# Optimization experiments

Measured on AMD Instinct MI355X. Metric: run time of the kernel, lower is better.

## Reference

```python
import jax, jax.numpy as jnp
import numpy as np

B, N, QD = 2, 4096, 512
HEADS, DIM_HEAD = 8, 64
INNER = HEADS * DIM_HEAD  # 512
SCALE = DIM_HEAD ** -0.5


def setup_inputs() -> dict:
    key = jax.random.key(0)
    ks = jax.random.split(key, 6)
    s = 0.02
    return {
        "x": jax.random.normal(ks[0], (B, N, QD), dtype=jnp.float32),
        "Wq": jax.random.normal(ks[1], (QD, INNER), dtype=jnp.float32) * s,
        "Wk": jax.random.normal(ks[2], (QD, INNER), dtype=jnp.float32) * s,
        "Wv": jax.random.normal(ks[3], (QD, INNER), dtype=jnp.float32) * s,
        "Wo": jax.random.normal(ks[4], (INNER, QD), dtype=jnp.float32) * s,
        "bo": jnp.zeros((QD,), dtype=jnp.float32),
    }


def reference(x, Wq, Wk, Wv, Wo, bo):
    # self-attention: context = x; mask = None; attention_sf = False
    q = x @ Wq  # [B, N, INNER]
    k = x @ Wk
    v = x @ Wv
    # split heads: [B, H, N, D]
    def split(t):
        return t.reshape(B, N, HEADS, DIM_HEAD).transpose(0, 2, 1, 3)
    q, k, v = split(q), split(k), split(v)
    # fp32 QK^T (ATTN_PRECISION='fp32' path)
    sim = jnp.einsum('bhid,bhjd->bhij', q.astype(jnp.float32), k.astype(jnp.float32)) * SCALE
    attn = jax.nn.softmax(sim, axis=-1)
    out = jnp.einsum('bhij,bhjd->bhid', attn, v)  # [B, H, N, D]
    out = out.transpose(0, 2, 1, 3).reshape(B, N, INNER)
    return out @ Wo + bo  # Dropout(p=0) is identity
```

## Files before the change

### kernel.cpp

```cpp
#include <hip/hip_runtime.h>
#include <hip/hip_bf16.h>


typedef __attribute__((ext_vector_type(8))) short short8;
typedef __attribute__((ext_vector_type(4))) float floatx4;

#define MFMA16(a, b, c) __builtin_amdgcn_mfma_f32_16x16x32_bf16((a), (b), (c), 0, 0, 0)

#if __has_builtin(__builtin_amdgcn_exp2f)
#define EXP2(x) __builtin_amdgcn_exp2f(x)
#else
#define EXP2(x) exp2f(x)
#endif

#define QSCALE 0.18033688011112042f

static __device__ __forceinline__ unsigned short f2b(float f) {
  unsigned int u = __float_as_uint(f);
  u += 0x7FFFu + ((u >> 16) & 1u);
  return (unsigned short)(u >> 16);
}

static __device__ __forceinline__ unsigned int pkb(float a, float b) {
  float2 t{a, b};
  __hip_bfloat162 h = __float22bfloat162_rn(t);
  union { __hip_bfloat162 h2; unsigned int u; } cv;
  cv.h2 = h;
  return cv.u;
}

static __device__ __forceinline__ void dma16(const unsigned short* g,
                                             unsigned short* l) {
  __builtin_amdgcn_global_load_lds(
      (const __attribute__((address_space(1))) unsigned int*)g,
      (__attribute__((address_space(3))) unsigned int*)l, 16, 0, 0);
}

__global__ __launch_bounds__(256) void prep_kernel(
    const float* __restrict__ Wq, const float* __restrict__ Wk,
    const float* __restrict__ Wv, const float* __restrict__ Wo,
    const float* __restrict__ x, unsigned short* __restrict__ wtq,
    unsigned short* __restrict__ wtk, unsigned short* __restrict__ wtv,
    unsigned short* __restrict__ wto, unsigned short* __restrict__ xb) {
  const int z = blockIdx.z;
  const int tid = threadIdx.x;
  if (z >= 4) {
    const int bid = (z - 4) * 256 + blockIdx.y * 16 + blockIdx.x;
    const int idx = (bid * 256 + tid) * 8;
    const float4 a = *(const float4*)(x + idx);
    const float4 b = *(const float4*)(x + idx + 4);
    unsigned int u[4] = {pkb(a.x, a.y), pkb(a.z, a.w), pkb(b.x, b.y),
                         pkb(b.z, b.w)};
    *(short8*)(xb + idx) = *(short8*)u;
    return;
  }
  const float* __restrict__ W = (z == 0) ? Wq : (z == 1) ? Wk : (z == 2) ? Wv : Wo;
  unsigned short* __restrict__ T = (z == 0) ? wtq : (z == 1) ? wtk : (z == 2) ? wtv : wto;
  const int k0 = blockIdx.x * 32, c0 = blockIdx.y * 32;
  __shared__ float Ts[32][33];
  const int r = tid >> 3, cc = (tid & 7) * 4;
  const float4 v = *(const float4*)(W + (k0 + r) * 512 + c0 + cc);
  Ts[r][cc] = v.x; Ts[r][cc + 1] = v.y; Ts[r][cc + 2] = v.z; Ts[r][cc + 3] = v.w;
  __syncthreads();
  const unsigned long long uu =
      (unsigned long long)pkb(Ts[cc][r], Ts[cc + 1][r]) |
      ((unsigned long long)pkb(Ts[cc + 2][r], Ts[cc + 3][r]) << 32);
  *(unsigned long long*)(T + (c0 + r) * 512 + k0 + cc) = uu;
}

__global__ __launch_bounds__(256) void qkv_fused_kernel(
    const unsigned short* __restrict__ xb, const unsigned short* __restrict__ wtq,
    const unsigned short* __restrict__ wtk,
    const unsigned short* __restrict__ wtv, unsigned short* __restrict__ qo,
    unsigned short* __restrict__ ko, unsigned short* __restrict__ vo) {
  const int m0 = blockIdx.x * 128;
  const int c0 = blockIdx.y * 32;
  __shared__ __align__(16) unsigned short As[2][128 * 64];
  __shared__ __align__(16) unsigned short Bs[2][3][32 * 64];
  const int tid = threadIdx.x;
  const int lane = tid & 63, w = tid >> 6;
  const int i = lane & 15, q = lane >> 4;
  const int sl = i & 7;
  const int dr = lane >> 3, dc = lane & 7;
  const int sch = (dc ^ dr) * 8;
  const unsigned short* ag = xb + (m0 + w * 32 + dr) * 512 + sch;
  const unsigned short* bg[3];
  bg[0] = wtq + (c0 + w * 8 + dr) * 512 + sch;
  bg[1] = wtk + (c0 + w * 8 + dr) * 512 + sch;
  bg[2] = wtv + (c0 + w * 8 + dr) * 512 + sch;

  floatx4 acc[3][2][2] = {};

#pragma unroll
  for (int p = 0; p < 4; ++p) dma16(ag + p * 8 * 512, &As[0][(w * 32 + p * 8) * 64]);
#pragma unroll
  for (int z = 0; z < 3; ++z) dma16(bg[z], &Bs[0][z][(w * 8) * 64]);
  __syncthreads();

  int buf = 0;
  for (int ks = 0; ks < 8; ++ks) {
    if (ks < 7) {
      const int k1 = (ks + 1) * 64;
#pragma unroll
      for (int p = 0; p < 4; ++p)
        dma16(ag + p * 8 * 512 + k1, &As[buf ^ 1][(w * 32 + p * 8) * 64]);
#pragma unroll
      for (int z = 0; z < 3; ++z)
        dma16(bg[z] + k1, &Bs[buf ^ 1][z][(w * 8) * 64]);
    }
#pragma unroll
    for (int kc = 0; kc < 2; ++kc) {
      short8 af[2];
#pragma unroll
      for (int t = 0; t < 2; ++t)
        af[t] = *(const short8*)&As[buf][(w * 32 + t * 16 + i) * 64 +
                                        (((kc * 4 + q) ^ sl) * 8)];
#pragma unroll
      for (int z = 0; z < 3; ++z)
#pragma unroll
        for (int g = 0; g < 2; ++g) {
          const short8 bf = *(const short8*)&Bs[buf][z][(g * 16 + i) * 64 +
                                                        (((kc * 4 + q) ^ sl) * 8)];
#pragma unroll
          for (int t = 0; t < 2; ++t)
            acc[z][t][g] = MFMA16(af[t], bf, acc[z][t][g]);
        }
    }
    __syncthreads();
    buf ^= 1;
  }
#pragma unroll
  for (int z = 0; z < 3; ++z)
#pragma unroll
    for (int t = 0; t < 2; ++t)
#pragma unroll
      for (int g = 0; g < 2; ++g) {
        const int col = c0 + g * 16 + i;
        const int h = col >> 6, d = col & 63;
        const int row0 = m0 + w * 32 + t * 16 + q * 4;
        const int b = row0 >> 12;
        const int n0 = row0 & 4095;
        if (z == 2) {
          unsigned int* dst =
              (unsigned int*)&vo[(((b * 8 + h) * 64 + d) << 12) + n0];
          dst[0] = pkb(acc[z][t][g][0], acc[z][t][g][1]);
          dst[1] = pkb(acc[z][t][g][2], acc[z][t][g][3]);
        } else {
          unsigned short* dst = (z == 0) ? qo : ko;
          const float sc = (z == 0) ? QSCALE : 1.0f;
#pragma unroll
          for (int r = 0; r < 4; ++r)
            dst[(((b * 8 + h) << 12) + (n0 + r)) * 64 + d] =
                f2b(acc[z][t][g][r] * sc);
        }
      }
}

__global__ __launch_bounds__(512, 4) void flash_kernel(
    const unsigned short* __restrict__ Q, const unsigned short* __restrict__ K,
    const unsigned short* __restrict__ Vt, unsigned short* __restrict__ O) {
  const int bh = blockIdx.x;
  const int m0 = blockIdx.y * 128;
  const int tid = threadIdx.x;
  const int lane = tid & 63, w = tid >> 6;
  const int i = lane & 15, q = lane >> 4;
  const int rt = w & 3;
  const int kg = w >> 2;
  const unsigned short* qp = Q + bh * (4096 * 64);
  const unsigned short* kp = K + bh * (4096 * 64);
  const unsigned short* vp = Vt + bh * (64 * 4096);

  __shared__ __align__(16) unsigned short SM[32768];
  unsigned short* Ks = SM + kg * 4096;
  unsigned short* Vs = SM + 8192 + kg * 4096;
  unsigned short* pw = SM + 16384 + w * 2048;

  const int srow = (tid & 255) >> 3;
  const int c0s = tid & 7;
  const int sw8 = (c0s ^ (srow & 7)) * 8;
  const unsigned short* kgp = kp + (kg * 2048 + srow) * 64 + c0s * 8;
  const unsigned short* vgp = vp + srow * 4096 + kg * 2048 + c0s * 8;

  short8 qf[2][2];
#pragma unroll
  for (int t = 0; t < 2; ++t)
#pragma unroll
    for (int kc = 0; kc < 2; ++kc)
      qf[t][kc] = *(const short8*)(qp + (m0 + rt * 32 + t * 16 + i) * 64 +
                                   kc * 32 + q * 8);

  floatx4 accO[2][4] = {};
  floatx4 accL[2] = {};
  short8 ones;
  {
    const short ov = (i == 0) ? (short)0x3F80 : (short)0;
#pragma unroll
    for (int j = 0; j < 8; ++j) ones[j] = ov;
  }
  const floatx4 zf = {0.f, 0.f, 0.f, 0.f};
  const int sl = i & 7;

  *(short8*)&Ks[srow * 64 + sw8] = *(const short8*)(kgp);
  *(short8*)&Ks[(srow + 32) * 64 + sw8] = *(const short8*)(kgp + 32 * 64);
  *(short8*)&Vs[srow * 64 + sw8] = *(const short8*)(vgp);
  *(short8*)&Vs[(srow + 32) * 64 + sw8] = *(const short8*)(vgp + 32 * 4096);
  __syncthreads();

  for (int jt = 0; jt < 32; ++jt) {
    short8 kn0, kn1, vn0, vn1;
    if (jt < 31) {
      kn0 = *(const short8*)(kgp + (jt + 1) * 4096);
      kn1 = *(const short8*)(kgp + (jt + 1) * 4096 + 32 * 64);
      vn0 = *(const short8*)(vgp + (jt + 1) * 64);
      vn1 = *(const short8*)(vgp + (jt + 1) * 64 + 32 * 4096);
    }
#pragma unroll
    for (int g = 0; g < 4; ++g) {
      const short8 kf0 = *(const short8*)(&Ks[(g * 16 + i) * 64 + (q ^ sl) * 8]);
      const short8 kf1 =
          *(const short8*)(&Ks[(g * 16 + i) * 64 + ((4 + q) ^ sl) * 8]);
#pragma unroll
      for (int t = 0; t < 2; ++t) {
        floatx4 s = MFMA16(kf0, qf[t][0], zf);
        s = MFMA16(kf1, qf[t][1], s);
        const float e0 = EXP2(s[0]), e1 = EXP2(s[1]);
        const float e2 = EXP2(s[2]), e3 = EXP2(s[3]);
        *(unsigned long long*)&pw[(t * 16 + i) * 64 +
                                  (((2 * g + (q >> 1)) ^ sl) * 8) +
                                  (q & 1) * 4] =
            (unsigned long long)pkb(e0, e1) |
            ((unsigned long long)pkb(e2, e3) << 32);
      }
    }
    short8 pf[2][2];
#pragma unroll
    for (int t = 0; t < 2; ++t) {
      pf[t][0] = *(const short8*)(pw + (t * 16 + i) * 64 + (q ^ sl) * 8);
      pf[t][1] = *(const short8*)(pw + (t * 16 + i) * 64 + ((4 + q) ^ sl) * 8);
      accL[t] = MFMA16(pf[t][0], ones, accL[t]);
      accL[t] = MFMA16(pf[t][1], ones, accL[t]);
    }
#pragma unroll
    for (int dg = 0; dg < 4; ++dg) {
      const short8 vf0 =
          *(const short8*)(&Vs[(dg * 16 + i) * 64 + (q ^ sl) * 8]);
      const short8 vf1 =
          *(const short8*)(&Vs[(dg * 16 + i) * 64 + ((4 + q) ^ sl) * 8]);
#pragma unroll
      for (int t = 0; t < 2; ++t) {
        accO[t][dg] = MFMA16(pf[t][0], vf0, accO[t][dg]);
        accO[t][dg] = MFMA16(pf[t][1], vf1, accO[t][dg]);
      }
    }
    __syncthreads();
    if (jt < 31) {
      *(short8*)&Ks[srow * 64 + sw8] = kn0;
      *(short8*)&Ks[(srow + 32) * 64 + sw8] = kn1;
      *(short8*)&Vs[srow * 64 + sw8] = vn0;
      *(short8*)&Vs[(srow + 32) * 64 + sw8] = vn1;
    }
    __syncthreads();
  }

  float* MB = (float*)SM;
  if (kg == 1) {
    float* dst = MB + (rt * 64 + lane) * 40;
#pragma unroll
    for (int t = 0; t < 2; ++t) {
#pragma unroll
      for (int dg = 0; dg < 4; ++dg)
#pragma unroll
        for (int r = 0; r < 4; ++r) dst[t * 16 + dg * 4 + r] = accO[t][dg][r];
#pragma unroll
      for (int r = 0; r < 4; ++r) dst[32 + t * 4 + r] = accL[t][r];
    }
  }
  __syncthreads();
  if (kg == 1) return;
  {
    const float* src = MB + (rt * 64 + lane) * 40;
#pragma unroll
    for (int t = 0; t < 2; ++t) {
#pragma unroll
      for (int dg = 0; dg < 4; ++dg)
#pragma unroll
        for (int r = 0; r < 4; ++r) accO[t][dg][r] += src[t * 16 + dg * 4 + r];
#pragma unroll
      for (int r = 0; r < 4; ++r) accL[t][r] += src[32 + t * 4 + r];
    }
  }

  const int b = bh >> 3, h = bh & 7;
#pragma unroll
  for (int t = 0; t < 2; ++t) {
    float inv[4];
#pragma unroll
    for (int r = 0; r < 4; ++r) {
      const float l = __shfl(accL[t][r], lane & 48, 64);
      inv[r] = 1.0f / l;
    }
#pragma unroll
    for (int dg = 0; dg < 4; ++dg)
#pragma unroll
      for (int r = 0; r < 4; ++r) {
        const int n = m0 + rt * 32 + t * 16 + q * 4 + r;
        const int col = h * 64 + dg * 16 + i;
        O[((b << 12) + n) * 512 + col] = f2b(accO[t][dg][r] * inv[r]);
      }
  }
}

__global__ __launch_bounds__(256) void out_proj_kernel(
    const unsigned short* __restrict__ A, const unsigned short* __restrict__ wto,
    const float* __restrict__ bo, float* __restrict__ out) {
  const int m0 = blockIdx.x * 64, c0 = blockIdx.y * 64;
  __shared__ __align__(16) unsigned short As[2][64 * 64];
  __shared__ __align__(16) unsigned short Bs[2][64 * 64];
  const int tid = threadIdx.x;
  const int lane = tid & 63, w = tid >> 6;
  const int i = lane & 15, q = lane >> 4;
  const int wy = w >> 1, wx = w & 1;
  const int sl = i & 7;
  const int dr = lane >> 3, dc = lane & 7;
  const int sch = (dc ^ dr) * 8;
  const unsigned short* ag = A + (m0 + w * 16 + dr) * 512 + sch;
  const unsigned short* bg = wto + (c0 + w * 16 + dr) * 512 + sch;

  floatx4 acc[2][2] = {};
#pragma unroll
  for (int p = 0; p < 2; ++p) {
    dma16(ag + p * 8 * 512, &As[0][(w * 16 + p * 8) * 64]);
    dma16(bg + p * 8 * 512, &Bs[0][(w * 16 + p * 8) * 64]);
  }
  __syncthreads();

  int buf = 0;
  for (int ks = 0; ks < 8; ++ks) {
    if (ks < 7) {
      const int k1 = (ks + 1) * 64;
#pragma unroll
      for (int p = 0; p < 2; ++p) {
        dma16(ag + p * 8 * 512 + k1, &As[buf ^ 1][(w * 16 + p * 8) * 64]);
        dma16(bg + p * 8 * 512 + k1, &Bs[buf ^ 1][(w * 16 + p * 8) * 64]);
      }
    }
#pragma unroll
    for (int kc = 0; kc < 2; ++kc) {
      short8 af[2], bfr[2];
#pragma unroll
      for (int t = 0; t < 2; ++t)
        af[t] = *(const short8*)&As[buf][(wy * 32 + t * 16 + i) * 64 +
                                        (((kc * 4 + q) ^ sl) * 8)];
#pragma unroll
      for (int g = 0; g < 2; ++g)
        bfr[g] = *(const short8*)&Bs[buf][(wx * 32 + g * 16 + i) * 64 +
                                          (((kc * 4 + q) ^ sl) * 8)];
#pragma unroll
      for (int t = 0; t < 2; ++t)
#pragma unroll
        for (int g = 0; g < 2; ++g) acc[t][g] = MFMA16(af[t], bfr[g], acc[t][g]);
    }
    __syncthreads();
    buf ^= 1;
  }
#pragma unroll
  for (int t = 0; t < 2; ++t)
#pragma unroll
    for (int g = 0; g < 2; ++g) {
      const int col = c0 + wx * 32 + g * 16 + i;
      const float bias = bo[col];
#pragma unroll
      for (int r = 0; r < 4; ++r) {
        const int row = m0 + wy * 32 + t * 16 + q * 4 + r;
        out[row * 512 + col] = acc[t][g][r] + bias;
      }
    }
}

extern "C" void kernel_launch(void* const* d_in, const int* in_sizes, int n_in,
                              void* d_out, int out_size, void* d_ws,
                              size_t ws_size, hipStream_t stream) {
  const float* x = (const float*)d_in[0];
  const float* Wq = (const float*)d_in[1];
  const float* Wk = (const float*)d_in[2];
  const float* Wv = (const float*)d_in[3];
  const float* Wo = (const float*)d_in[4];
  const float* bo = (const float*)d_in[5];
  float* out = (float*)d_out;

  const size_t tsz = (size_t)16 * 4096 * 64;
  unsigned short* qws = (unsigned short*)d_ws;
  unsigned short* kws = qws + tsz;
  unsigned short* vws = kws + tsz;
  unsigned short* ows = vws + tsz;
  unsigned short* wtq = ows + tsz;
  unsigned short* wtk = wtq + 512 * 512;
  unsigned short* wtv = wtk + 512 * 512;
  unsigned short* wto = wtv + 512 * 512;
  unsigned short* xb = wto + 512 * 512;

  prep_kernel<<<dim3(16, 16, 12), 256, 0, stream>>>(Wq, Wk, Wv, Wo, x, wtq,
                                                    wtk, wtv, wto, xb);
  qkv_fused_kernel<<<dim3(64, 16), 256, 0, stream>>>(xb, wtq, wtk, wtv, qws,
                                                     kws, vws);
  flash_kernel<<<dim3(16, 32), 512, 0, stream>>>(qws, kws, vws, ows);
  out_proj_kernel<<<dim3(128, 8), 256, 0, stream>>>(ows, wto, bo, out);
}
```

Before: 192.8 us.

## Switch flash attention to 32x32 MFMA with register-resident P via permlane swaps

Rewrites the attention inner loop to use 32x32x16 bf16 MFMAs instead of 16x16x32. S is computed transposed (K as A operand), so the exponentiated scores can be repacked in registers with v_permlane32_swap and fed directly as the A operand of the PV MFMA, removing the per-wave LDS round trip for P. Row sums are now taken with VALU adds instead of extra MFMAs against a ones vector, and shared memory shrinks. The trade-off is higher register pressure from 16-wide accumulators and a more intricate output-row mapping.

```diff
diff --git a/kernel.cpp b/kernel.cpp
--- a/kernel.cpp
+++ b/kernel.cpp
@@ -4,8 +4,10 @@
 
 typedef __attribute__((ext_vector_type(8))) short short8;
 typedef __attribute__((ext_vector_type(4))) float floatx4;
+typedef __attribute__((ext_vector_type(16))) float floatx16;
 
 #define MFMA16(a, b, c) __builtin_amdgcn_mfma_f32_16x16x32_bf16((a), (b), (c), 0, 0, 0)
+#define MFMA32(a, b, c) __builtin_amdgcn_mfma_f32_32x32x16_bf16((a), (b), (c), 0, 0, 0)
 
 #if __has_builtin(__builtin_amdgcn_exp2f)
 #define EXP2(x) __builtin_amdgcn_exp2f(x)
@@ -163,17 +165,16 @@
   const int m0 = blockIdx.y * 128;
   const int tid = threadIdx.x;
   const int lane = tid & 63, w = tid >> 6;
-  const int i = lane & 15, q = lane >> 4;
+  const int ql = lane & 31, hi = lane >> 5;
   const int rt = w & 3;
   const int kg = w >> 2;
   const unsigned short* qp = Q + bh * (4096 * 64);
   const unsigned short* kp = K + bh * (4096 * 64);
   const unsigned short* vp = Vt + bh * (64 * 4096);
 
-  __shared__ __align__(16) unsigned short SM[32768];
+  __shared__ __align__(16) unsigned short SM[20480];
   unsigned short* Ks = SM + kg * 4096;
   unsigned short* Vs = SM + 8192 + kg * 4096;
-  unsigned short* pw = SM + 16384 + w * 2048;
 
   const int srow = (tid & 255) >> 3;
   const int c0s = tid & 7;
@@ -181,24 +182,16 @@
   const unsigned short* kgp = kp + (kg * 2048 + srow) * 64 + c0s * 8;
   const unsigned short* vgp = vp + srow * 4096 + kg * 2048 + c0s * 8;
 
-  short8 qf[2][2];
-#pragma unroll
-  for (int t = 0; t < 2; ++t)
-#pragma unroll
-    for (int kc = 0; kc < 2; ++kc)
-      qf[t][kc] = *(const short8*)(qp + (m0 + rt * 32 + t * 16 + i) * 64 +
-                                   kc * 32 + q * 8);
-
-  floatx4 accO[2][4] = {};
-  floatx4 accL[2] = {};
-  short8 ones;
+  short8 qf[4];
   {
-    const short ov = (i == 0) ? (short)0x3F80 : (short)0;
-#pragma unroll
-    for (int j = 0; j < 8; ++j) ones[j] = ov;
-  }
-  const floatx4 zf = {0.f, 0.f, 0.f, 0.f};
-  const int sl = i & 7;
+    const unsigned short* qrp = qp + (m0 + rt * 32 + ql) * 64 + hi * 8;
+#pragma unroll
+    for (int ks = 0; ks < 4; ++ks) qf[ks] = *(const short8*)(qrp + ks * 16);
+  }
+
+  floatx16 accO[2] = {};
+  float accLp = 0.f;
+  const int sx = ql & 7;
 
   *(short8*)&Ks[srow * 64 + sw8] = *(const short8*)(kgp);
   *(short8*)&Ks[(srow + 32) * 64 + sw8] = *(const short8*)(kgp + 32 * 64);
@@ -214,44 +207,47 @@
       vn0 = *(const short8*)(vgp + (jt + 1) * 64);
       vn1 = *(const short8*)(vgp + (jt + 1) * 64 + 32 * 4096);
     }
-#pragma unroll
-    for (int g = 0; g < 4; ++g) {
-      const short8 kf0 = *(const short8*)(&Ks[(g * 16 + i) * 64 + (q ^ sl) * 8]);
-      const short8 kf1 =
-          *(const short8*)(&Ks[(g * 16 + i) * 64 + ((4 + q) ^ sl) * 8]);
-#pragma unroll
-      for (int t = 0; t < 2; ++t) {
-        floatx4 s = MFMA16(kf0, qf[t][0], zf);
-        s = MFMA16(kf1, qf[t][1], s);
-        const float e0 = EXP2(s[0]), e1 = EXP2(s[1]);
-        const float e2 = EXP2(s[2]), e3 = EXP2(s[3]);
-        *(unsigned long long*)&pw[(t * 16 + i) * 64 +
-                                  (((2 * g + (q >> 1)) ^ sl) * 8) +
-                                  (q & 1) * 4] =
-            (unsigned long long)pkb(e0, e1) |
-            ((unsigned long long)pkb(e2, e3) << 32);
-      }
-    }
-    short8 pf[2][2];
-#pragma unroll
-    for (int t = 0; t < 2; ++t) {
-      pf[t][0] = *(const short8*)(pw + (t * 16 + i) * 64 + (q ^ sl) * 8);
-      pf[t][1] = *(const short8*)(pw + (t * 16 + i) * 64 + ((4 + q) ^ sl) * 8);
-      accL[t] = MFMA16(pf[t][0], ones, accL[t]);
-      accL[t] = MFMA16(pf[t][1], ones, accL[t]);
-    }
-#pragma unroll
-    for (int dg = 0; dg < 4; ++dg) {
-      const short8 vf0 =
-          *(const short8*)(&Vs[(dg * 16 + i) * 64 + (q ^ sl) * 8]);
-      const short8 vf1 =
-          *(const short8*)(&Vs[(dg * 16 + i) * 64 + ((4 + q) ^ sl) * 8]);
-#pragma unroll
-      for (int t = 0; t < 2; ++t) {
-        accO[t][dg] = MFMA16(pf[t][0], vf0, accO[t][dg]);
-        accO[t][dg] = MFMA16(pf[t][1], vf1, accO[t][dg]);
-      }
-    }
+
+    short8 pa[4];
+#pragma unroll
+    for (int kt = 0; kt < 2; ++kt) {
+      floatx16 c;
+#pragma unroll
+      for (int j = 0; j < 16; ++j) c[j] = 0.0f;
+#pragma unroll
+      for (int ks = 0; ks < 4; ++ks) {
+        const short8 kf = *(const short8*)&Ks[(kt * 32 + ql) * 64 +
+                                             (((2 * ks + hi) ^ sx) * 8)];
+        c = MFMA32(kf, qf[ks], c);
+      }
+      float e[16];
+#pragma unroll
+      for (int j = 0; j < 16; ++j) e[j] = EXP2(c[j]);
+      accLp += (((e[0] + e[1]) + (e[2] + e[3])) +
+                ((e[4] + e[5]) + (e[6] + e[7]))) +
+               (((e[8] + e[9]) + (e[10] + e[11])) +
+                ((e[12] + e[13]) + (e[14] + e[15])));
+#pragma unroll
+      for (int s2 = 0; s2 < 2; ++s2) {
+        unsigned int a0 = pkb(e[8 * s2 + 0], e[8 * s2 + 1]);
+        unsigned int c1 = pkb(e[8 * s2 + 2], e[8 * s2 + 3]);
+        unsigned int b0 = pkb(e[8 * s2 + 4], e[8 * s2 + 5]);
+        unsigned int d1 = pkb(e[8 * s2 + 6], e[8 * s2 + 7]);
+        asm("v_permlane32_swap_b32 %0, %1" : "+v"(a0), "+v"(b0));
+        asm("v_permlane32_swap_b32 %0, %1" : "+v"(c1), "+v"(d1));
+        union { unsigned int u[4]; short8 s; } cv;
+        cv.u[0] = a0; cv.u[1] = c1; cv.u[2] = b0; cv.u[3] = d1;
+        pa[kt * 2 + s2] = cv.s;
+      }
+    }
+#pragma unroll
+    for (int dt = 0; dt < 2; ++dt)
+#pragma unroll
+      for (int ks2 = 0; ks2 < 4; ++ks2) {
+        const short8 vf = *(const short8*)&Vs[(dt * 32 + ql) * 64 +
+                                              (((2 * ks2 + hi) ^ sx) * 8)];
+        accO[dt] = MFMA32(pa[ks2], vf, accO[dt]);
+      }
     __syncthreads();
     if (jt < 31) {
       *(short8*)&Ks[srow * 64 + sw8] = kn0;
@@ -266,47 +262,35 @@
   if (kg == 1) {
     float* dst = MB + (rt * 64 + lane) * 40;
 #pragma unroll
-    for (int t = 0; t < 2; ++t) {
-#pragma unroll
-      for (int dg = 0; dg < 4; ++dg)
-#pragma unroll
-        for (int r = 0; r < 4; ++r) dst[t * 16 + dg * 4 + r] = accO[t][dg][r];
-#pragma unroll
-      for (int r = 0; r < 4; ++r) dst[32 + t * 4 + r] = accL[t][r];
-    }
+    for (int dt = 0; dt < 2; ++dt)
+#pragma unroll
+      for (int r = 0; r < 16; ++r) dst[dt * 16 + r] = accO[dt][r];
+    dst[32] = accLp;
   }
   __syncthreads();
   if (kg == 1) return;
   {
     const float* src = MB + (rt * 64 + lane) * 40;
 #pragma unroll
-    for (int t = 0; t < 2; ++t) {
-#pragma unroll
-      for (int dg = 0; dg < 4; ++dg)
-#pragma unroll
-        for (int r = 0; r < 4; ++r) accO[t][dg][r] += src[t * 16 + dg * 4 + r];
-#pragma unroll
-      for (int r = 0; r < 4; ++r) accL[t][r] += src[32 + t * 4 + r];
-    }
-  }
-
+    for (int dt = 0; dt < 2; ++dt)
+#pragma unroll
+      for (int r = 0; r < 16; ++r) accO[dt][r] += src[dt * 16 + r];
+    accLp += src[32];
+  }
+
+  const float Lfull = accLp + __shfl(accLp, lane ^ 32, 64);
+  const float invL = 1.0f / Lfull;
   const int b = bh >> 3, h = bh & 7;
 #pragma unroll
-  for (int t = 0; t < 2; ++t) {
-    float inv[4];
-#pragma unroll
-    for (int r = 0; r < 4; ++r) {
-      const float l = __shfl(accL[t][r], lane & 48, 64);
-      inv[r] = 1.0f / l;
-    }
-#pragma unroll
-    for (int dg = 0; dg < 4; ++dg)
-#pragma unroll
-      for (int r = 0; r < 4; ++r) {
-        const int n = m0 + rt * 32 + t * 16 + q * 4 + r;
-        const int col = h * 64 + dg * 16 + i;
-        O[((b << 12) + n) * 512 + col] = f2b(accO[t][dg][r] * inv[r]);
-      }
+  for (int r = 0; r < 16; ++r) {
+    const int qrow = (r & 3) + 8 * (r >> 2) + 4 * hi;
+    const float iv = __shfl(invL, qrow, 64);
+    const int n = m0 + rt * 32 + qrow;
+#pragma unroll
+    for (int dt = 0; dt < 2; ++dt) {
+      const int col = h * 64 + dt * 32 + ql;
+      O[((b << 12) + n) * 512 + col] = f2b(accO[dt][r] * iv);
+    }
   }
 }
 
```

New measurement: 195.9 us. Within noise of the previous version (+1.6%).
